# Performance work log

Measured on AMD Instinct MI355X. Metric: run time of the kernel, lower is better.

Reference implementation:

```python
import jax, jax.numpy as jnp
import numpy as np

N, SEQ_LEN, HORIZON, F_IN, EMBED, HIDDEN, LAYERS = 4096, 168, 24, 32, 32, 64, 2
G4 = 4 * HIDDEN
# NOTE: original torch code calls nn.LSTM per-step WITHOUT carrying hidden state,
# so each step's LSTM starts from (h0=0, c0=0): W_hh contributes nothing, only b_hh.

def setup_inputs() -> dict:
    key = jax.random.key(0)
    ks = jax.random.split(key, 12)
    s = 0.1
    return {
        "X": jax.random.normal(ks[0], (N, SEQ_LEN, F_IN), jnp.float32),
        "y": jax.random.normal(ks[1], (N, SEQ_LEN), jnp.float32),
        "Xf": jax.random.normal(ks[2], (N, HORIZON, F_IN), jnp.float32),
        "W_embed": jax.random.normal(ks[3], (EMBED, 1), jnp.float32) * s,
        "b_embed": jax.random.normal(ks[4], (EMBED,), jnp.float32) * s,
        "W_ih": jax.random.normal(ks[5], (LAYERS, G4, EMBED + F_IN), jnp.float32) * s,  # layer1 in-dim == HIDDEN == EMBED+F_IN
        "b_ih": jax.random.normal(ks[6], (LAYERS, G4), jnp.float32) * s,
        "b_hh": jax.random.normal(ks[7], (LAYERS, G4), jnp.float32) * s,
        "W_mu": jax.random.normal(ks[8], (1, HIDDEN), jnp.float32) * s,
        "b_mu": jax.random.normal(ks[9], (1,), jnp.float32) * s,
        "W_sigma": jax.random.normal(ks[10], (1, HIDDEN), jnp.float32) * s,
        "b_sigma": jax.random.normal(ks[11], (1,), jnp.float32) * s,
    }


def reference(X, y, Xf, W_embed, b_embed, W_ih, b_ih, b_hh, W_mu, b_mu, W_sigma, b_sigma):
    num_ts = X.shape[0]
    T = SEQ_LEN + HORIZON
    Xall = jnp.concatenate([X, Xf], axis=1)  # (N, T, F_IN)
    y_pad = jnp.concatenate([y, jnp.zeros((num_ts, HORIZON), y.dtype)], axis=1)  # (N, T)
    use_y = jnp.arange(T) < SEQ_LEN  # teacher-forced region

    def step(carry, inputs):
        x_s, y_s, use = inputs  # (N, F_IN), (N,), scalar bool
        ynext = jnp.where(use, y_s[:, None], carry)  # (N, 1)
        yembed = ynext @ W_embed.T + b_embed  # (N, EMBED)
        h = jnp.concatenate([x_s, yembed], axis=1)  # (N, F_IN+EMBED)
        for l in range(LAYERS):  # single LSTM step from zero state per layer
            gates = h @ W_ih[l].T + b_ih[l] + b_hh[l]  # (N, 4H); torch gate order i,f,g,o
            i_g, f_g, g_g, o_g = jnp.split(gates, 4, axis=1)
            c = jax.nn.sigmoid(i_g) * jnp.tanh(g_g)  # f * c0 term vanishes (c0 = 0)
            h = jax.nn.sigmoid(o_g) * jnp.tanh(c)
        h = jax.nn.relu(h)
        mu = h @ W_mu.T + b_mu  # (N, 1)
        sigma = jax.nn.softplus(h @ W_sigma.T + b_sigma) + 1e-6  # log(1+exp(.)) + eps
        lik = (2.0 * np.pi * sigma ** 2) ** (-0.5) * jnp.exp(-((ynext - mu) ** 2) / (2.0 * sigma ** 2))
        return lik, (lik[:, 0], mu[:, 0], sigma[:, 0])

    carry0 = jnp.zeros((num_ts, 1), X.dtype)
    xs = (jnp.swapaxes(Xall, 0, 1), y_pad.T, use_y)
    _, (lik_t, mu_t, sigma_t) = jax.lax.scan(step, carry0, xs)  # each (T, N)
    ypred = lik_t.T[:, SEQ_LEN - 1: SEQ_LEN + HORIZON - 1]  # (N, HORIZON)
    return ypred, mu_t.T, sigma_t.T
```

## Files before the change

kernel.cpp:

```cpp
#include <hip/hip_runtime.h>
#include <math.h>

#define N_TS 4096
#define SEQ  168
#define HOR  24
#define T_ALL 192
#define F_INP 32
#define HID  64
#define NROW 192
#define L2E  1.44269504089f

typedef _Float16 half8  __attribute__((ext_vector_type(8)));
typedef _Float16 half4  __attribute__((ext_vector_type(4)));
typedef float    floatx4 __attribute__((ext_vector_type(4)));

__device__ __forceinline__ float fexp(float x)  { return __expf(x); }
__device__ __forceinline__ float ex2(float x)   { return __builtin_amdgcn_exp2f(x); }
__device__ __forceinline__ float frcp(float x)  { return __builtin_amdgcn_rcpf(x); }
__device__ __forceinline__ float softplus_(float x) { return (x > 15.0f) ? x : __logf(1.0f + fexp(x)); }

__device__ __forceinline__ float lstm_h(float ip, float gp, float op) {
    const float Ei = ex2(ip);
    const float Eg = ex2(gp);
    const float cc = (1.0f - Eg) * frcp((1.0f + Ei) * (1.0f + Eg));
    const float Ec = ex2(cc * (-2.0f * L2E));
    const float Eo = ex2(op);
    return (1.0f - Ec) * frcp((1.0f + Ec) * (1.0f + Eo));
}

__device__ __forceinline__ half8 cvt8(const float4 a, const float4 b) {
    half8 v;
    v[0]=(_Float16)a.x; v[1]=(_Float16)a.y; v[2]=(_Float16)a.z; v[3]=(_Float16)a.w;
    v[4]=(_Float16)b.x; v[5]=(_Float16)b.y; v[6]=(_Float16)b.z; v[7]=(_Float16)b.w;
    return v;
}

__global__ __launch_bounds__(256) void prep(
    const float* __restrict__ W_ih, const float* __restrict__ b_ih,
    const float* __restrict__ b_hh,
    _Float16* __restrict__ W16f, float* __restrict__ bsum)
{
    const int idx = blockIdx.x * 256 + threadIdx.x;
    for (int i = idx; i < 2 * 8 * NROW * 8; i += gridDim.x * 256) {
        const int kp  = i & 7;
        const int row = (i >> 3) % NROW;
        const int kb  = ((i >> 3) / NROW) & 7;
        const int l   = i / (8 * NROW * 8);
        const int sr  = (row < 64) ? row : row + 64;
        const float sc = (row >= 64 && row < 128) ? (-2.0f * L2E) : (-L2E);
        W16f[i] = (_Float16)(W_ih[(l * 256 + sr) * HID + kb * 8 + kp] * sc);
    }
    for (int i = idx; i < 2 * NROW; i += gridDim.x * 256) {
        const int r = i % NROW;
        const int l = i / NROW;
        const int sr = (r < 64) ? r : r + 64;
        const float sc = (r >= 64 && r < 128) ? (-2.0f * L2E) : (-L2E);
        bsum[i] = (b_ih[l * 256 + sr] + b_hh[l * 256 + sr]) * sc;
    }
}

__global__ __launch_bounds__(256, 5) void cellsA(
    const float* __restrict__ X,
    const float* __restrict__ y,
    const float* __restrict__ W_embed,
    const float* __restrict__ b_embed,
    const _Float16* __restrict__ W16f,
    const float* __restrict__ bsum,
    const float* __restrict__ W_mu,
    const float* __restrict__ b_mu,
    const float* __restrict__ W_sigma,
    const float* __restrict__ b_sigma,
    float* __restrict__ out,
    float* __restrict__ lik167)
{
    __shared__ __align__(16) _Float16 Wl[NROW * HID];
    __shared__ __align__(16) _Float16 Hx[4][16 * 64];
    const int tid  = threadIdx.x;
    const int w    = tid >> 6;
    const int lane = tid & 63;
    const int quad = lane >> 4;
    const int ln   = lane & 15;
    const int cid0 = blockIdx.x * 64 + w * 16;
    const int cid  = cid0 + ln;

    half8 afr0, afr1;
    {
        const float* xp = X + (size_t)cid * F_INP + quad * 8;
        const float4 xa = *(const float4*)xp;
        const float4 xb = *(const float4*)(xp + 4);
        afr0 = cvt8(xa, xb);
        const float yv = y[cid];
        const float4 wa = *(const float4*)(W_embed + quad * 8);
        const float4 wb = *(const float4*)(W_embed + quad * 8 + 4);
        const float4 ba = *(const float4*)(b_embed + quad * 8);
        const float4 bb = *(const float4*)(b_embed + quad * 8 + 4);
        afr1[0]=(_Float16)fmaf(yv, wa.x, ba.x); afr1[1]=(_Float16)fmaf(yv, wa.y, ba.y);
        afr1[2]=(_Float16)fmaf(yv, wa.z, ba.z); afr1[3]=(_Float16)fmaf(yv, wa.w, ba.w);
        afr1[4]=(_Float16)fmaf(yv, wb.x, bb.x); afr1[5]=(_Float16)fmaf(yv, wb.y, bb.y);
        afr1[6]=(_Float16)fmaf(yv, wb.z, bb.z); afr1[7]=(_Float16)fmaf(yv, wb.w, bb.w);
    }

    #pragma unroll
    for (int c = 0; c < 6; ++c) {
        const int off = (c * 256 + tid) * 8;
        *(half8*)(Wl + off) = *(const half8*)(W16f + off);
    }
    __syncthreads();

    _Float16* hrow = Hx[w];
    {
        const _Float16* bp = Wl + quad * 1536 + ln * 8;
        #pragma unroll
        for (int jt = 0; jt < 4; ++jt) {
            const float bi = bsum[jt * 16 + ln];
            const float bg = bsum[(4 + jt) * 16 + ln];
            const float bo = bsum[(8 + jt) * 16 + ln];
            floatx4 ai = (floatx4){bi, bi, bi, bi};
            floatx4 ag = (floatx4){bg, bg, bg, bg};
            floatx4 ao = (floatx4){bo, bo, bo, bo};
            ai = __builtin_amdgcn_mfma_f32_16x16x32_f16(afr0, *(const half8*)(bp + jt * 128),            ai, 0, 0, 0);
            ai = __builtin_amdgcn_mfma_f32_16x16x32_f16(afr1, *(const half8*)(bp + jt * 128 + 6144),     ai, 0, 0, 0);
            ag = __builtin_amdgcn_mfma_f32_16x16x32_f16(afr0, *(const half8*)(bp + (4 + jt) * 128),      ag, 0, 0, 0);
            ag = __builtin_amdgcn_mfma_f32_16x16x32_f16(afr1, *(const half8*)(bp + (4 + jt) * 128 + 6144), ag, 0, 0, 0);
            ao = __builtin_amdgcn_mfma_f32_16x16x32_f16(afr0, *(const half8*)(bp + (8 + jt) * 128),      ao, 0, 0, 0);
            ao = __builtin_amdgcn_mfma_f32_16x16x32_f16(afr1, *(const half8*)(bp + (8 + jt) * 128 + 6144), ao, 0, 0, 0);
            #pragma unroll
            for (int r = 0; r < 4; ++r) {
                const float hh = lstm_h(ai[r], ag[r], ao[r]);
                const int row = quad * 4 + r;
                const int col = jt * 16 + ln;
                hrow[row * 64 + (((col >> 3) ^ (row & 7)) << 3) + (col & 7)] = (_Float16)hh;
            }
        }
    }

    const half8 a0 = *(const half8*)(hrow + ln * 64 + ((quad ^ (ln & 7)) << 3));
    const half8 a1 = *(const half8*)(hrow + ln * 64 + (((4 + quad) ^ (ln & 7)) << 3));

    __syncthreads();
    #pragma unroll
    for (int c = 0; c < 6; ++c) {
        const int off = (c * 256 + tid) * 8;
        *(half8*)(Wl + off) = *(const half8*)(W16f + 12288 + off);
    }
    __syncthreads();

    float hfin[4][4];
    {
        const _Float16* bp = Wl + quad * 1536 + ln * 8;
        #pragma unroll
        for (int jt = 0; jt < 4; ++jt) {
            const float bi = bsum[NROW + jt * 16 + ln];
            const float bg = bsum[NROW + (4 + jt) * 16 + ln];
            const float bo = bsum[NROW + (8 + jt) * 16 + ln];
            floatx4 ai = (floatx4){bi, bi, bi, bi};
            floatx4 ag = (floatx4){bg, bg, bg, bg};
            floatx4 ao = (floatx4){bo, bo, bo, bo};
            ai = __builtin_amdgcn_mfma_f32_16x16x32_f16(a0, *(const half8*)(bp + jt * 128),            ai, 0, 0, 0);
            ai = __builtin_amdgcn_mfma_f32_16x16x32_f16(a1, *(const half8*)(bp + jt * 128 + 6144),     ai, 0, 0, 0);
            ag = __builtin_amdgcn_mfma_f32_16x16x32_f16(a0, *(const half8*)(bp + (4 + jt) * 128),      ag, 0, 0, 0);
            ag = __builtin_amdgcn_mfma_f32_16x16x32_f16(a1, *(const half8*)(bp + (4 + jt) * 128 + 6144), ag, 0, 0, 0);
            ao = __builtin_amdgcn_mfma_f32_16x16x32_f16(a0, *(const half8*)(bp + (8 + jt) * 128),      ao, 0, 0, 0);
            ao = __builtin_amdgcn_mfma_f32_16x16x32_f16(a1, *(const half8*)(bp + (8 + jt) * 128 + 6144), ao, 0, 0, 0);
            #pragma unroll
            for (int r = 0; r < 4; ++r)
                hfin[jt][r] = lstm_h(ai[r], ag[r], ao[r]);
        }
    }

    float wmu[4], wsg[4];
    #pragma unroll
    for (int jt = 0; jt < 4; ++jt) {
        wmu[jt] = W_mu[jt * 16 + ln];
        wsg[jt] = W_sigma[jt * 16 + ln];
    }
    const float bmu = b_mu[0], bsg = b_sigma[0];
    float* mu_out = out + (size_t)N_TS * HOR;
    float* sg_out = mu_out + (size_t)N_TS * T_ALL;

    #pragma unroll
    for (int r = 0; r < 4; ++r) {
        float pm = 0.f, ps = 0.f;
        #pragma unroll
        for (int jt = 0; jt < 4; ++jt) {
            const float hr = fmaxf(hfin[jt][r], 0.0f);
            pm = fmaf(hr, wmu[jt], pm);
            ps = fmaf(hr, wsg[jt], ps);
        }
        #pragma unroll
        for (int off = 1; off < 16; off <<= 1) {
            pm += __shfl_xor(pm, off, 64);
            ps += __shfl_xor(ps, off, 64);
        }
        if (ln == 0) {
            const int cid2 = cid0 + quad * 4 + r;
            const int n = cid2 / SEQ;
            const int t = cid2 - n * SEQ;
            const float mu = pm + bmu;
            const float sg = softplus_(ps + bsg) + 1e-6f;
            mu_out[(size_t)n * T_ALL + t] = mu;
            sg_out[(size_t)n * T_ALL + t] = sg;
            if (t == SEQ - 1) {
                const float yv = y[cid2];
                const float d  = yv - mu;
                const float is = frcp(sg);
                const float lik = 0.39894228040143267f * is * fexp(-0.5f * d * d * is * is);
                out[(size_t)n * HOR] = lik;
                lik167[n] = lik;
            }
        }
    }
}

__global__ __launch_bounds__(64, 1) void cellsB(
    const float* __restrict__ Xf,
    const _Float16* __restrict__ W16f,
    const float* __restrict__ bsum,
    const float* __restrict__ W_embed,
    const float* __restrict__ b_embed,
    const float* __restrict__ W_mu,
    const float* __restrict__ b_mu,
    const float* __restrict__ W_sigma,
    const float* __restrict__ b_sigma,
    float* __restrict__ out,
    const float* __restrict__ lik167)
{
    __shared__ __align__(16) _Float16 W2l[12288];
    __shared__ __align__(16) float    b2l[NROW];
    __shared__ __align__(16) _Float16 slab[16 * 72];
    const int lane = threadIdx.x;
    const int quad = lane >> 4;
    const int ln   = lane & 15;
    const int n0   = blockIdx.x * 16;

    #pragma unroll
    for (int c = 0; c < 24; ++c) {
        const int off = (c * 64 + lane) * 8;
        *(half8*)(W2l + off) = *(const half8*)(W16f + 12288 + off);
    }
    #pragma unroll
    for (int c = 0; c < 3; ++c)
        b2l[c * 64 + lane] = bsum[NROW + c * 64 + lane];
    __builtin_amdgcn_s_waitcnt(0);

    half8 W1f[12][2];
    #pragma unroll
    for (int nt = 0; nt < 12; ++nt)
        #pragma unroll
        for (int kf = 0; kf < 2; ++kf)
            W1f[nt][kf] = *(const half8*)(W16f + ((size_t)(kf * 4 + quad) * NROW + nt * 16 + ln) * 8);
    float4 b1v[12];
    #pragma unroll
    for (int nt = 0; nt < 12; ++nt)
        b1v[nt] = *(const float4*)(bsum + nt * 16 + quad * 4);
    float we[8], be[8];
    #pragma unroll
    for (int e = 0; e < 8; ++e) {
        we[e] = W_embed[quad * 8 + e];
        be[e] = b_embed[quad * 8 + e];
    }
    float4 wmuv[4], wsgv[4];
    #pragma unroll
    for (int jt = 0; jt < 4; ++jt) {
        wmuv[jt] = *(const float4*)(W_mu + jt * 16 + quad * 4);
        wsgv[jt] = *(const float4*)(W_sigma + jt * 16 + quad * 4);
    }
    const float bmu = b_mu[0], bsg = b_sigma[0];

    float yv = lik167[n0 + ln];

    float* mu_out = out + (size_t)N_TS * HOR;
    float* sg_out = mu_out + (size_t)N_TS * T_ALL;

    const float* xp = Xf + (size_t)(n0 + ln) * HOR * F_INP + quad * 8;
    float4 xa = *(const float4*)xp;
    float4 xb = *(const float4*)(xp + 4);

    #pragma unroll 1
    for (int s = 0; s < HOR; ++s) {
        const half8 xf0 = cvt8(xa, xb);
        if (s < HOR - 1) {
            xa = *(const float4*)(xp + (s + 1) * F_INP);
            xb = *(const float4*)(xp + (s + 1) * F_INP + 4);
        }
        half8 xf1;
        #pragma unroll
        for (int e = 0; e < 8; ++e)
            xf1[e] = (_Float16)fmaf(yv, we[e], be[e]);

        floatx4 acc[12];
        #pragma unroll
        for (int nt = 0; nt < 12; ++nt) {
            acc[nt] = (floatx4){b1v[nt].x, b1v[nt].y, b1v[nt].z, b1v[nt].w};
            acc[nt] = __builtin_amdgcn_mfma_f32_16x16x32_f16(W1f[nt][0], xf0, acc[nt], 0, 0, 0);
            acc[nt] = __builtin_amdgcn_mfma_f32_16x16x32_f16(W1f[nt][1], xf1, acc[nt], 0, 0, 0);
        }

        #pragma unroll
        for (int jt = 0; jt < 4; ++jt) {
            half4 hp;
            #pragma unroll
            for (int r = 0; r < 4; ++r)
                hp[r] = (_Float16)lstm_h(acc[jt][r], acc[4 + jt][r], acc[8 + jt][r]);
            *(half4*)(&slab[ln * 72 + jt * 16 + quad * 4]) = hp;
        }
        const half8 a0 = *(const half8*)(&slab[ln * 72 + quad * 8]);
        const half8 a1 = *(const half8*)(&slab[ln * 72 + 32 + quad * 8]);

        #pragma unroll
        for (int nt = 0; nt < 12; ++nt) {
            const floatx4 bi = *(const floatx4*)(b2l + nt * 16 + quad * 4);
            floatx4 a = bi;
            a = __builtin_amdgcn_mfma_f32_16x16x32_f16(
                    *(const half8*)(W2l + ((size_t)quad * NROW + nt * 16 + ln) * 8), a0, a, 0, 0, 0);
            a = __builtin_amdgcn_mfma_f32_16x16x32_f16(
                    *(const half8*)(W2l + ((size_t)(4 + quad) * NROW + nt * 16 + ln) * 8), a1, a, 0, 0, 0);
            acc[nt] = a;
        }

        float pm = 0.f, ps = 0.f;
        #pragma unroll
        for (int jt = 0; jt < 4; ++jt)
        #pragma unroll
        for (int r = 0; r < 4; ++r) {
            const float hh = lstm_h(acc[jt][r], acc[4 + jt][r], acc[8 + jt][r]);
            const float hr = fmaxf(hh, 0.0f);
            pm = fmaf(hr, ((const float*)&wmuv[jt])[r], pm);
            ps = fmaf(hr, ((const float*)&wsgv[jt])[r], ps);
        }
        pm += __shfl_xor(pm, 16, 64);  pm += __shfl_xor(pm, 32, 64);
        ps += __shfl_xor(ps, 16, 64);  ps += __shfl_xor(ps, 32, 64);

        const float mu = pm + bmu;
        const float sg = softplus_(ps + bsg) + 1e-6f;
        const float d  = yv - mu;
        const float is = frcp(sg);
        const float lik = 0.39894228040143267f * is * fexp(-0.5f * d * d * is * is);

        if (quad == 0) {
            const int nn = n0 + ln;
            const int t  = SEQ + s;
            mu_out[(size_t)nn * T_ALL + t] = mu;
            sg_out[(size_t)nn * T_ALL + t] = sg;
            if (s < HOR - 1) out[(size_t)nn * HOR + s + 1] = lik;
        }
        yv = lik;
    }
}

extern "C" void kernel_launch(void* const* d_in, const int* in_sizes, int n_in,
                              void* d_out, int out_size, void* d_ws, size_t ws_size,
                              hipStream_t stream) {
    const float* X       = (const float*)d_in[0];
    const float* y       = (const float*)d_in[1];
    const float* Xf      = (const float*)d_in[2];
    const float* W_embed = (const float*)d_in[3];
    const float* b_embed = (const float*)d_in[4];
    const float* W_ih    = (const float*)d_in[5];
    const float* b_ih    = (const float*)d_in[6];
    const float* b_hh    = (const float*)d_in[7];
    const float* W_mu    = (const float*)d_in[8];
    const float* b_mu    = (const float*)d_in[9];
    const float* W_sigma = (const float*)d_in[10];
    const float* b_sigma = (const float*)d_in[11];

    float* out = (float*)d_out;
    float*     lik167 = (float*)d_ws;
    _Float16*  W16f   = (_Float16*)((char*)d_ws + 16384);
    float*     bsum   = (float*)((char*)d_ws + 16384 + 49152);

    prep<<<96, 256, 0, stream>>>(W_ih, b_ih, b_hh, W16f, bsum);

    cellsA<<<(N_TS * SEQ) / 64, 256, 0, stream>>>(
        X, y, W_embed, b_embed, W16f, bsum,
        W_mu, b_mu, W_sigma, b_sigma, out, lik167);

    cellsB<<<N_TS / 16, 64, 0, stream>>>(
        Xf, W16f, bsum, W_embed, b_embed,
        W_mu, b_mu, W_sigma, b_sigma, out, lik167);
}
```

Measured before the change: 282.4 us.

## Fuse teacher-forced and horizon kernels into one launch, recomputing step 167 locally

Merges the parallel teacher-forced cell kernel and the sequential horizon kernel into one launch. The first 256 blocks run the horizon recurrence and now recompute the last teacher-forced step themselves instead of reading it from a workspace buffer. The remaining blocks do the parallel cells concurrently, so the serial horizon tail overlaps with the bulk work and the inter-kernel dependency is gone. In exchange, a shared-memory union sized for both layer weight sets raises LDS use per block and lowers launch bounds from 5 to 3, cutting occupancy for the parallel cells. Horizon blocks also idle three of their four waves.

```diff
diff --git a/kernel.cpp b/kernel.cpp
--- a/kernel.cpp
+++ b/kernel.cpp
@@ -8,6 +8,7 @@
 #define F_INP 32
 #define HID  64
 #define NROW 192
+#define NB_B (N_TS / 16)
 #define L2E  1.44269504089f
 
 typedef _Float16 half8  __attribute__((ext_vector_type(8)));
@@ -59,9 +60,10 @@
     }
 }
 
-__global__ __launch_bounds__(256, 5) void cellsA(
+__global__ __launch_bounds__(256, 3) void fused(
     const float* __restrict__ X,
     const float* __restrict__ y,
+    const float* __restrict__ Xf,
     const float* __restrict__ W_embed,
     const float* __restrict__ b_embed,
     const _Float16* __restrict__ W16f,
@@ -70,17 +72,137 @@
     const float* __restrict__ b_mu,
     const float* __restrict__ W_sigma,
     const float* __restrict__ b_sigma,
-    float* __restrict__ out,
-    float* __restrict__ lik167)
+    float* __restrict__ out)
 {
-    __shared__ __align__(16) _Float16 Wl[NROW * HID];
-    __shared__ __align__(16) _Float16 Hx[4][16 * 64];
-    const int tid  = threadIdx.x;
+    __shared__ union {
+        struct { _Float16 Wl[12288]; _Float16 Hx[4][1024]; } A;
+        struct { _Float16 W1[12288]; _Float16 W2[12288];
+                 _Float16 slab[16 * 72]; float b1[NROW]; float b2[NROW]; } B;
+    } sh;
+
+    const int tid = threadIdx.x;
+    float* mu_out = out + (size_t)N_TS * HOR;
+    float* sg_out = mu_out + (size_t)N_TS * T_ALL;
+
+    if (blockIdx.x < NB_B) {
+        if (tid >= 64) return;
+        const int lane = tid;
+        const int quad = lane >> 4;
+        const int ln   = lane & 15;
+        const int n0   = blockIdx.x * 16;
+
+        #pragma unroll
+        for (int c = 0; c < 48; ++c) {
+            const int off = (c * 64 + lane) * 8;
+            *(half8*)(sh.B.W1 + off) = *(const half8*)(W16f + off);
+        }
+        #pragma unroll
+        for (int c = 0; c < 6; ++c)
+            sh.B.b1[c * 64 + lane] = bsum[c * 64 + lane];
+        __builtin_amdgcn_s_waitcnt(0);
+
+        float we[8], be[8];
+        #pragma unroll
+        for (int e = 0; e < 8; ++e) {
+            we[e] = W_embed[quad * 8 + e];
+            be[e] = b_embed[quad * 8 + e];
+        }
+        float4 wmuv[4], wsgv[4];
+        #pragma unroll
+        for (int jt = 0; jt < 4; ++jt) {
+            wmuv[jt] = *(const float4*)(W_mu + jt * 16 + quad * 4);
+            wsgv[jt] = *(const float4*)(W_sigma + jt * 16 + quad * 4);
+        }
+        const float bmu = b_mu[0], bsg = b_sigma[0];
+
+        const float* xfp = Xf + (size_t)(n0 + ln) * HOR * F_INP + quad * 8;
+        float yv = y[(size_t)(n0 + ln) * SEQ + (SEQ - 1)];
+        float4 xa, xb;
+        {
+            const float* xp = X + ((size_t)(n0 + ln) * SEQ + (SEQ - 1)) * F_INP + quad * 8;
+            xa = *(const float4*)xp;
+            xb = *(const float4*)(xp + 4);
+        }
+
+        #pragma unroll 1
+        for (int st = 0; st <= HOR; ++st) {
+            const half8 xf0 = cvt8(xa, xb);
+            if (st < HOR) {
+                xa = *(const float4*)(xfp + st * F_INP);
+                xb = *(const float4*)(xfp + st * F_INP + 4);
+            }
+            half8 xf1;
+            #pragma unroll
+            for (int e = 0; e < 8; ++e)
+                xf1[e] = (_Float16)fmaf(yv, we[e], be[e]);
+
+            floatx4 acc[12];
+            #pragma unroll
+            for (int nt = 0; nt < 12; ++nt) {
+                acc[nt] = *(const floatx4*)(sh.B.b1 + nt * 16 + quad * 4);
+                acc[nt] = __builtin_amdgcn_mfma_f32_16x16x32_f16(
+                    *(const half8*)(sh.B.W1 + ((size_t)quad * NROW + nt * 16 + ln) * 8), xf0, acc[nt], 0, 0, 0);
+                acc[nt] = __builtin_amdgcn_mfma_f32_16x16x32_f16(
+                    *(const half8*)(sh.B.W1 + ((size_t)(4 + quad) * NROW + nt * 16 + ln) * 8), xf1, acc[nt], 0, 0, 0);
+            }
+
+            #pragma unroll
+            for (int jt = 0; jt < 4; ++jt) {
+                half4 hp;
+                #pragma unroll
+                for (int r = 0; r < 4; ++r)
+                    hp[r] = (_Float16)lstm_h(acc[jt][r], acc[4 + jt][r], acc[8 + jt][r]);
+                *(half4*)(&sh.B.slab[ln * 72 + jt * 16 + quad * 4]) = hp;
+            }
+            const half8 a0 = *(const half8*)(&sh.B.slab[ln * 72 + quad * 8]);
+            const half8 a1 = *(const half8*)(&sh.B.slab[ln * 72 + 32 + quad * 8]);
+
+            #pragma unroll
+            for (int nt = 0; nt < 12; ++nt) {
+                floatx4 a = *(const floatx4*)(sh.B.b2 + nt * 16 + quad * 4);
+                a = __builtin_amdgcn_mfma_f32_16x16x32_f16(
+                    *(const half8*)(sh.B.W2 + ((size_t)quad * NROW + nt * 16 + ln) * 8), a0, a, 0, 0, 0);
+                a = __builtin_amdgcn_mfma_f32_16x16x32_f16(
+                    *(const half8*)(sh.B.W2 + ((size_t)(4 + quad) * NROW + nt * 16 + ln) * 8), a1, a, 0, 0, 0);
+                acc[nt] = a;
+            }
+
+            float pm = 0.f, ps = 0.f;
+            #pragma unroll
+            for (int jt = 0; jt < 4; ++jt)
+            #pragma unroll
+            for (int r = 0; r < 4; ++r) {
+                const float hh = lstm_h(acc[jt][r], acc[4 + jt][r], acc[8 + jt][r]);
+                const float hr = fmaxf(hh, 0.0f);
+                pm = fmaf(hr, ((const float*)&wmuv[jt])[r], pm);
+                ps = fmaf(hr, ((const float*)&wsgv[jt])[r], ps);
+            }
+            pm += __shfl_xor(pm, 16, 64);  pm += __shfl_xor(pm, 32, 64);
+            ps += __shfl_xor(ps, 16, 64);  ps += __shfl_xor(ps, 32, 64);
+
+            const float mu = pm + bmu;
+            const float sg = softplus_(ps + bsg) + 1e-6f;
+            const float d  = yv - mu;
+            const float is = frcp(sg);
+            const float lik = 0.39894228040143267f * is * fexp(-0.5f * d * d * is * is);
+
+            if (st > 0 && quad == 0) {
+                const int nn = n0 + ln;
+                const int t  = SEQ + st - 1;
+                mu_out[(size_t)nn * T_ALL + t] = mu;
+                sg_out[(size_t)nn * T_ALL + t] = sg;
+                if (st < HOR) out[(size_t)nn * HOR + st] = lik;
+            }
+            yv = lik;
+        }
+        return;
+    }
+
     const int w    = tid >> 6;
     const int lane = tid & 63;
     const int quad = lane >> 4;
     const int ln   = lane & 15;
-    const int cid0 = blockIdx.x * 64 + w * 16;
+    const int cid0 = (blockIdx.x - NB_B) * 64 + w * 16;
     const int cid  = cid0 + ln;
 
     half8 afr0, afr1;
@@ -103,13 +225,13 @@
     #pragma unroll
     for (int c = 0; c < 6; ++c) {
         const int off = (c * 256 + tid) * 8;
-        *(half8*)(Wl + off) = *(const half8*)(W16f + off);
+        *(half8*)(sh.A.Wl + off) = *(const half8*)(W16f + off);
     }
     __syncthreads();
 
-    _Float16* hrow = Hx[w];
+    _Float16* hrow = sh.A.Hx[w];
     {
-        const _Float16* bp = Wl + quad * 1536 + ln * 8;
+        const _Float16* bp = sh.A.Wl + quad * 1536 + ln * 8;
         #pragma unroll
         for (int jt = 0; jt < 4; ++jt) {
             const float bi = bsum[jt * 16 + ln];
@@ -118,11 +240,11 @@
             floatx4 ai = (floatx4){bi, bi, bi, bi};
             floatx4 ag = (floatx4){bg, bg, bg, bg};
             floatx4 ao = (floatx4){bo, bo, bo, bo};
-            ai = __builtin_amdgcn_mfma_f32_16x16x32_f16(afr0, *(const half8*)(bp + jt * 128),            ai, 0, 0, 0);
-            ai = __builtin_amdgcn_mfma_f32_16x16x32_f16(afr1, *(const half8*)(bp + jt * 128 + 6144),     ai, 0, 0, 0);
-            ag = __builtin_amdgcn_mfma_f32_16x16x32_f16(afr0, *(const half8*)(bp + (4 + jt) * 128),      ag, 0, 0, 0);
+            ai = __builtin_amdgcn_mfma_f32_16x16x32_f16(afr0, *(const half8*)(bp + jt * 128),              ai, 0, 0, 0);
+            ai = __builtin_amdgcn_mfma_f32_16x16x32_f16(afr1, *(const half8*)(bp + jt * 128 + 6144),       ai, 0, 0, 0);
+            ag = __builtin_amdgcn_mfma_f32_16x16x32_f16(afr0, *(const half8*)(bp + (4 + jt) * 128),        ag, 0, 0, 0);
             ag = __builtin_amdgcn_mfma_f32_16x16x32_f16(afr1, *(const half8*)(bp + (4 + jt) * 128 + 6144), ag, 0, 0, 0);
-            ao = __builtin_amdgcn_mfma_f32_16x16x32_f16(afr0, *(const half8*)(bp + (8 + jt) * 128),      ao, 0, 0, 0);
+            ao = __builtin_amdgcn_mfma_f32_16x16x32_f16(afr0, *(const half8*)(bp + (8 + jt) * 128),        ao, 0, 0, 0);
             ao = __builtin_amdgcn_mfma_f32_16x16x32_f16(afr1, *(const half8*)(bp + (8 + jt) * 128 + 6144), ao, 0, 0, 0);
             #pragma unroll
             for (int r = 0; r < 4; ++r) {
@@ -141,13 +263,13 @@
     #pragma unroll
     for (int c = 0; c < 6; ++c) {
         const int off = (c * 256 + tid) * 8;
-        *(half8*)(Wl + off) = *(const half8*)(W16f + 12288 + off);
+        *(half8*)(sh.A.Wl + off) = *(const half8*)(W16f + 12288 + off);
     }
     __syncthreads();
 
     float hfin[4][4];
     {
-        const _Float16* bp = Wl + quad * 1536 + ln * 8;
+        const _Float16* bp = sh.A.Wl + quad * 1536 + ln * 8;
         #pragma unroll
         for (int jt = 0; jt < 4; ++jt) {
             const float bi = bsum[NROW + jt * 16 + ln];
@@ -156,11 +278,11 @@
             floatx4 ai = (floatx4){bi, bi, bi, bi};
             floatx4 ag = (floatx4){bg, bg, bg, bg};
             floatx4 ao = (floatx4){bo, bo, bo, bo};
-            ai = __builtin_amdgcn_mfma_f32_16x16x32_f16(a0, *(const half8*)(bp + jt * 128),            ai, 0, 0, 0);
-            ai = __builtin_amdgcn_mfma_f32_16x16x32_f16(a1, *(const half8*)(bp + jt * 128 + 6144),     ai, 0, 0, 0);
-            ag = __builtin_amdgcn_mfma_f32_16x16x32_f16(a0, *(const half8*)(bp + (4 + jt) * 128),      ag, 0, 0, 0);
+            ai = __builtin_amdgcn_mfma_f32_16x16x32_f16(a0, *(const half8*)(bp + jt * 128),              ai, 0, 0, 0);
+            ai = __builtin_amdgcn_mfma_f32_16x16x32_f16(a1, *(const half8*)(bp + jt * 128 + 6144),       ai, 0, 0, 0);
+            ag = __builtin_amdgcn_mfma_f32_16x16x32_f16(a0, *(const half8*)(bp + (4 + jt) * 128),        ag, 0, 0, 0);
             ag = __builtin_amdgcn_mfma_f32_16x16x32_f16(a1, *(const half8*)(bp + (4 + jt) * 128 + 6144), ag, 0, 0, 0);
-            ao = __builtin_amdgcn_mfma_f32_16x16x32_f16(a0, *(const half8*)(bp + (8 + jt) * 128),      ao, 0, 0, 0);
+            ao = __builtin_amdgcn_mfma_f32_16x16x32_f16(a0, *(const half8*)(bp + (8 + jt) * 128),        ao, 0, 0, 0);
             ao = __builtin_amdgcn_mfma_f32_16x16x32_f16(a1, *(const half8*)(bp + (8 + jt) * 128 + 6144), ao, 0, 0, 0);
             #pragma unroll
             for (int r = 0; r < 4; ++r)
@@ -175,8 +297,6 @@
         wsg[jt] = W_sigma[jt * 16 + ln];
     }
     const float bmu = b_mu[0], bsg = b_sigma[0];
-    float* mu_out = out + (size_t)N_TS * HOR;
-    float* sg_out = mu_out + (size_t)N_TS * T_ALL;
 
     #pragma unroll
     for (int r = 0; r < 4; ++r) {
@@ -206,145 +326,8 @@
                 const float is = frcp(sg);
                 const float lik = 0.39894228040143267f * is * fexp(-0.5f * d * d * is * is);
                 out[(size_t)n * HOR] = lik;
-                lik167[n] = lik;
-            }
-        }
-    }
-}
-
-__global__ __launch_bounds__(64, 1) void cellsB(
-    const float* __restrict__ Xf,
-    const _Float16* __restrict__ W16f,
-    const float* __restrict__ bsum,
-    const float* __restrict__ W_embed,
-    const float* __restrict__ b_embed,
-    const float* __restrict__ W_mu,
-    const float* __restrict__ b_mu,
-    const float* __restrict__ W_sigma,
-    const float* __restrict__ b_sigma,
-    float* __restrict__ out,
-    const float* __restrict__ lik167)
-{
-    __shared__ __align__(16) _Float16 W2l[12288];
-    __shared__ __align__(16) float    b2l[NROW];
-    __shared__ __align__(16) _Float16 slab[16 * 72];
-    const int lane = threadIdx.x;
-    const int quad = lane >> 4;
-    const int ln   = lane & 15;
-    const int n0   = blockIdx.x * 16;
-
-    #pragma unroll
-    for (int c = 0; c < 24; ++c) {
-        const int off = (c * 64 + lane) * 8;
-        *(half8*)(W2l + off) = *(const half8*)(W16f + 12288 + off);
-    }
-    #pragma unroll
-    for (int c = 0; c < 3; ++c)
-        b2l[c * 64 + lane] = bsum[NROW + c * 64 + lane];
-    __builtin_amdgcn_s_waitcnt(0);
-
-    half8 W1f[12][2];
-    #pragma unroll
-    for (int nt = 0; nt < 12; ++nt)
-        #pragma unroll
-        for (int kf = 0; kf < 2; ++kf)
-            W1f[nt][kf] = *(const half8*)(W16f + ((size_t)(kf * 4 + quad) * NROW + nt * 16 + ln) * 8);
-    float4 b1v[12];
-    #pragma unroll
-    for (int nt = 0; nt < 12; ++nt)
-        b1v[nt] = *(const float4*)(bsum + nt * 16 + quad * 4);
-    float we[8], be[8];
-    #pragma unroll
-    for (int e = 0; e < 8; ++e) {
-        we[e] = W_embed[quad * 8 + e];
-        be[e] = b_embed[quad * 8 + e];
-    }
-    float4 wmuv[4], wsgv[4];
-    #pragma unroll
-    for (int jt = 0; jt < 4; ++jt) {
-        wmuv[jt] = *(const float4*)(W_mu + jt * 16 + quad * 4);
-        wsgv[jt] = *(const float4*)(W_sigma + jt * 16 + quad * 4);
-    }
-    const float bmu = b_mu[0], bsg = b_sigma[0];
-
-    float yv = lik167[n0 + ln];
-
-    float* mu_out = out + (size_t)N_TS * HOR;
-    float* sg_out = mu_out + (size_t)N_TS * T_ALL;
-
-    const float* xp = Xf + (size_t)(n0 + ln) * HOR * F_INP + quad * 8;
-    float4 xa = *(const float4*)xp;
-    float4 xb = *(const float4*)(xp + 4);
-
-    #pragma unroll 1
-    for (int s = 0; s < HOR; ++s) {
-        const half8 xf0 = cvt8(xa, xb);
-        if (s < HOR - 1) {
-            xa = *(const float4*)(xp + (s + 1) * F_INP);
-            xb = *(const float4*)(xp + (s + 1) * F_INP + 4);
-        }
-        half8 xf1;
-        #pragma unroll
-        for (int e = 0; e < 8; ++e)
-            xf1[e] = (_Float16)fmaf(yv, we[e], be[e]);
-
-        floatx4 acc[12];
-        #pragma unroll
-        for (int nt = 0; nt < 12; ++nt) {
-            acc[nt] = (floatx4){b1v[nt].x, b1v[nt].y, b1v[nt].z, b1v[nt].w};
-            acc[nt] = __builtin_amdgcn_mfma_f32_16x16x32_f16(W1f[nt][0], xf0, acc[nt], 0, 0, 0);
-            acc[nt] = __builtin_amdgcn_mfma_f32_16x16x32_f16(W1f[nt][1], xf1, acc[nt], 0, 0, 0);
-        }
-
-        #pragma unroll
-        for (int jt = 0; jt < 4; ++jt) {
-            half4 hp;
-            #pragma unroll
-            for (int r = 0; r < 4; ++r)
-                hp[r] = (_Float16)lstm_h(acc[jt][r], acc[4 + jt][r], acc[8 + jt][r]);
-            *(half4*)(&slab[ln * 72 + jt * 16 + quad * 4]) = hp;
-        }
-        const half8 a0 = *(const half8*)(&slab[ln * 72 + quad * 8]);
-        const half8 a1 = *(const half8*)(&slab[ln * 72 + 32 + quad * 8]);
-
-        #pragma unroll
-        for (int nt = 0; nt < 12; ++nt) {
-            const floatx4 bi = *(const floatx4*)(b2l + nt * 16 + quad * 4);
-            floatx4 a = bi;
-            a = __builtin_amdgcn_mfma_f32_16x16x32_f16(
-                    *(const half8*)(W2l + ((size_t)quad * NROW + nt * 16 + ln) * 8), a0, a, 0, 0, 0);
-            a = __builtin_amdgcn_mfma_f32_16x16x32_f16(
-                    *(const half8*)(W2l + ((size_t)(4 + quad) * NROW + nt * 16 + ln) * 8), a1, a, 0, 0, 0);
-            acc[nt] = a;
-        }
-
-        float pm = 0.f, ps = 0.f;
-        #pragma unroll
-        for (int jt = 0; jt < 4; ++jt)
-        #pragma unroll
-        for (int r = 0; r < 4; ++r) {
-            const float hh = lstm_h(acc[jt][r], acc[4 + jt][r], acc[8 + jt][r]);
-            const float hr = fmaxf(hh, 0.0f);
-            pm = fmaf(hr, ((const float*)&wmuv[jt])[r], pm);
-            ps = fmaf(hr, ((const float*)&wsgv[jt])[r], ps);
-        }
-        pm += __shfl_xor(pm, 16, 64);  pm += __shfl_xor(pm, 32, 64);
-        ps += __shfl_xor(ps, 16, 64);  ps += __shfl_xor(ps, 32, 64);
-
-        const float mu = pm + bmu;
-        const float sg = softplus_(ps + bsg) + 1e-6f;
-        const float d  = yv - mu;
-        const float is = frcp(sg);
-        const float lik = 0.39894228040143267f * is * fexp(-0.5f * d * d * is * is);
-
-        if (quad == 0) {
-            const int nn = n0 + ln;
-            const int t  = SEQ + s;
-            mu_out[(size_t)nn * T_ALL + t] = mu;
-            sg_out[(size_t)nn * T_ALL + t] = sg;
-            if (s < HOR - 1) out[(size_t)nn * HOR + s + 1] = lik;
-        }
-        yv = lik;
+            }
+        }
     }
 }
 
@@ -365,17 +348,12 @@
     const float* b_sigma = (const float*)d_in[11];
 
     float* out = (float*)d_out;
-    float*     lik167 = (float*)d_ws;
-    _Float16*  W16f   = (_Float16*)((char*)d_ws + 16384);
-    float*     bsum   = (float*)((char*)d_ws + 16384 + 49152);
+    _Float16*  W16f = (_Float16*)d_ws;
+    float*     bsum = (float*)((char*)d_ws + 49152);
 
     prep<<<96, 256, 0, stream>>>(W_ih, b_ih, b_hh, W16f, bsum);
 
-    cellsA<<<(N_TS * SEQ) / 64, 256, 0, stream>>>(
-        X, y, W_embed, b_embed, W16f, bsum,
-        W_mu, b_mu, W_sigma, b_sigma, out, lik167);
-
-    cellsB<<<N_TS / 16, 64, 0, stream>>>(
-        Xf, W16f, bsum, W_embed, b_embed,
-        W_mu, b_mu, W_sigma, b_sigma, out, lik167);
-}
+    fused<<<NB_B + (N_TS * SEQ) / 64, 256, 0, stream>>>(
+        X, y, Xf, W_embed, b_embed, W16f, bsum,
+        W_mu, b_mu, W_sigma, b_sigma, out);
+}
```

After: 289.3 us. 1.02x slower.
